# Optimization experiments

Measured on AMD Instinct MI355X. Metric: run time of the kernel, lower is better.

## Reference

```python
import jax, jax.numpy as jnp
import numpy as np
from jax import lax

D_MODEL = 1024
STATE_DIM = 32
GROUPS = 8
GROUP_DIM = D_MODEL // GROUPS
DT_MIN = 0.001
DT_MAX = 0.1
EPS = 1e-6


def setup_inputs() -> dict:
    key = jax.random.key(0)
    ks = jax.random.split(key, 6)
    B, T = 4, 4096
    u = jax.random.normal(ks[0], (B, T, D_MODEL), dtype=jnp.float32)
    state = jnp.zeros((B, GROUPS, STATE_DIM), dtype=jnp.float32)
    A_log = jax.random.normal(ks[1], (GROUPS, STATE_DIM), dtype=jnp.float32) * 0.02
    B_param = jax.random.normal(ks[2], (GROUPS, STATE_DIM, GROUP_DIM), dtype=jnp.float32) * 0.02
    C = jax.random.normal(ks[3], (GROUPS, GROUP_DIM, STATE_DIM), dtype=jnp.float32) * 0.02
    Dp = jnp.zeros((GROUPS, GROUP_DIM), dtype=jnp.float32)
    dt_logit = jnp.zeros((GROUPS,), dtype=jnp.float32)
    return {"u": u, "state": state, "A_log": A_log, "B_param": B_param,
            "C": C, "Dp": Dp, "dt_logit": dt_logit}


def reference(u, state, A_log, B_param, C, Dp, dt_logit):
    Bsz, T, Dm = u.shape
    A = -jax.nn.softplus(A_log)                                  # [G,N]
    dt = DT_MIN + (DT_MAX - DT_MIN) * jax.nn.sigmoid(dt_logit)   # [G]
    dt_g = dt[:, None]                                           # [G,1]
    Abar = jnp.exp(A * dt_g)                                     # [G,N]
    # (exp(A dt) - 1)/A, stable for small |A|
    frac = jnp.where(jnp.abs(A) > EPS, (Abar - 1.0) / A,
                     jnp.broadcast_to(dt_g, A.shape))            # [G,N]
    Bbar = frac[..., None] * B_param                             # [G,N,gd]

    u_g = u.reshape(Bsz, T, GROUPS, GROUP_DIM)                   # [B,T,G,gd]
    # precompute input injections for all timesteps, then scan the LTI recurrence
    Bu = jnp.einsum('btgi,gni->btgn', u_g, Bbar)                 # [B,T,G,N]
    Bu_t = jnp.moveaxis(Bu, 1, 0)                                # [T,B,G,N]

    def step(s, bu):
        s = s * Abar + bu                                        # [B,G,N]
        return s, s

    s_final, states = lax.scan(step, state, Bu_t)                # states: [T,B,G,N]
    Cs = jnp.einsum('tbgn,gdn->btgd', states, C)                 # [B,T,G,gd]
    y = (Cs + Dp * u_g).reshape(Bsz, T, Dm)                      # [B,T,D]
    return y, s_final
```

## Files before the change

### kernel.cpp

```cpp
#include <hip/hip_runtime.h>
#include <hip/hip_bf16.h>

#define DM 1024
#define SD 32
#define NG 8
#define GD 128
#define BS 4
#define TT 4096
#define CL 64
#define NC (TT/CL)

typedef __attribute__((ext_vector_type(8))) short short8;
typedef __attribute__((ext_vector_type(4))) float f32x4;

#define WS_POWA  0
#define WS_STL   65536
#define WS_CARRY (WS_STL + 8388608)
#define WS_PAL   (WS_CARRY + 262144)

__device__ __forceinline__ unsigned short f2bf(float f) {
  __hip_bfloat16 h = __float2bfloat16(f);
  return __builtin_bit_cast(unsigned short, h);
}
__device__ __forceinline__ float bf2f(unsigned short h) {
  return __uint_as_float(((unsigned)h) << 16);
}
__device__ __forceinline__ float softplus_f(float x) {
  return (x > 20.f) ? x : log1pf(expf(x));
}
__device__ __forceinline__ short8 pack8(float4 a, float4 b) {
  short8 h;
  h[0]=(short)f2bf(a.x); h[1]=(short)f2bf(a.y); h[2]=(short)f2bf(a.z); h[3]=(short)f2bf(a.w);
  h[4]=(short)f2bf(b.x); h[5]=(short)f2bf(b.y); h[6]=(short)f2bf(b.z); h[7]=(short)f2bf(b.w);
  return h;
}

__global__ __launch_bounds__(64) void ka_bu_scan(const float* __restrict__ u,
                                                 const float* __restrict__ A_log,
                                                 const float* __restrict__ B_param,
                                                 const float* __restrict__ dt_logit,
                                                 unsigned char* __restrict__ ws) {
  const int bx = blockIdx.x;
  const int c = bx & (NC - 1);
  const int g = (bx >> 6) & (NG - 1);
  const int b = bx >> 9;
  const int l = threadIdx.x;
  const int lr = l & 15, lh = l >> 4;

  const float dtg = 0.001f + 0.099f * (1.f / (1.f + expf(-dt_logit[g])));

  float fracv[2];
  #pragma unroll
  for (int nt = 0; nt < 2; ++nt) {
    int n = nt * 16 + lr;
    float A = -softplus_f(A_log[g * SD + n]);
    float a = expf(A * dtg);
    fracv[nt] = (fabsf(A) > 1e-6f) ? (a - 1.f) / A : dtg;
  }
  float a_scan;
  {
    float A = -softplus_f(A_log[g * SD + (l & 31)]);
    a_scan = expf(A * dtg);
  }

  const float* bp = B_param + (size_t)g * SD * GD;
  short8 bfr[4][2];
  #pragma unroll
  for (int kt = 0; kt < 4; ++kt)
    #pragma unroll
    for (int nt = 0; nt < 2; ++nt) {
      const float* p = bp + (size_t)(nt * 16 + lr) * GD + kt * 32 + lh * 8;
      float4 v0 = *(const float4*)p;
      float4 v1 = *(const float4*)(p + 4);
      float s = fracv[nt];
      v0.x*=s; v0.y*=s; v0.z*=s; v0.w*=s;
      v1.x*=s; v1.y*=s; v1.z*=s; v1.w*=s;
      bfr[kt][nt] = pack8(v0, v1);
    }

  const float* up = u + ((size_t)b * TT + (size_t)c * CL) * DM + g * GD;
  float4 ub[2][4][2];
  #pragma unroll
  for (int kt = 0; kt < 2; ++kt)
    #pragma unroll
    for (int m = 0; m < 4; ++m) {
      const float* p = up + (size_t)(m * 16 + lr) * DM + kt * 32 + lh * 8;
      ub[kt][m][0] = *(const float4*)p;
      ub[kt][m][1] = *(const float4*)(p + 4);
    }

  f32x4 acc[4][2];
  #pragma unroll
  for (int m = 0; m < 4; ++m)
    #pragma unroll
    for (int nt = 0; nt < 2; ++nt)
      #pragma unroll
      for (int j = 0; j < 4; ++j) acc[m][nt][j] = 0.f;

  #pragma unroll
  for (int kt = 0; kt < 4; ++kt) {
    short8 af[4];
    #pragma unroll
    for (int m = 0; m < 4; ++m)
      af[m] = pack8(ub[kt & 1][m][0], ub[kt & 1][m][1]);
    if (kt < 2) {
      #pragma unroll
      for (int m = 0; m < 4; ++m) {
        const float* p = up + (size_t)(m * 16 + lr) * DM + (kt + 2) * 32 + lh * 8;
        ub[kt & 1][m][0] = *(const float4*)p;
        ub[kt & 1][m][1] = *(const float4*)(p + 4);
      }
    }
    #pragma unroll
    for (int m = 0; m < 4; ++m)
      #pragma unroll
      for (int nt = 0; nt < 2; ++nt)
        acc[m][nt] = __builtin_amdgcn_mfma_f32_16x16x32_bf16(af[m], bfr[kt][nt], acc[m][nt], 0, 0, 0);
  }

  __shared__ __align__(16) float sBu[CL * 33];
  __shared__ __align__(16) unsigned short sSt[CL * SD];
  #pragma unroll
  for (int m = 0; m < 4; ++m)
    #pragma unroll
    for (int nt = 0; nt < 2; ++nt)
      #pragma unroll
      for (int j = 0; j < 4; ++j) {
        int t = m * 16 + lh * 4 + j;
        sBu[t * 33 + (nt * 16 + lr)] = acc[m][nt][j];
      }
  __syncthreads();

  float* carry = (float*)(ws + WS_CARRY);
  if (l < SD) {
    float s = 0.f;
    #pragma unroll
    for (int t = 0; t < CL; ++t) {
      s = fmaf(s, a_scan, sBu[t * 33 + l]);
      sSt[t * SD + l] = f2bf(s);
    }
    carry[((b * NG + g) * NC + c) * SD + l] = s;
  }
  __syncthreads();

  unsigned short* stg = (unsigned short*)(ws + WS_STL) + ((size_t)((b * NC + c) * NG + g)) * CL * SD;
  #pragma unroll
  for (int p = 0; p < 4; ++p) {
    int off = (p * 64 + l) * 8;
    *(short8*)(stg + off) = *(short8*)(sSt + off);
  }

  if (b == 0 && c == 0 && l < SD) {
    float* powA = (float*)(ws + WS_POWA);
    float* powAL = (float*)(ws + WS_PAL);
    float p = 1.f;
    #pragma unroll
    for (int t = 0; t < CL; ++t) {
      p *= a_scan;
      powA[(g * CL + t) * SD + l] = p;
    }
    float aL = p;
    float q = 1.f;
    #pragma unroll
    for (int j = 0; j < CL; ++j) {
      powAL[(g * CL + j) * SD + l] = q;
      q *= aL;
    }
  }
}

__global__ __launch_bounds__(128) void kb_y(const float* __restrict__ u,
                                            const float* __restrict__ state0,
                                            const float* __restrict__ C,
                                            const float* __restrict__ Dp,
                                            unsigned char* __restrict__ ws,
                                            float* __restrict__ y,
                                            float* __restrict__ sfin) {
  const int bx = blockIdx.x;
  const int c = bx & (NC - 1);
  const int g = (bx >> 6) & (NG - 1);
  const int b = bx >> 9;
  const int tid = threadIdx.x;
  const int w = tid >> 6;
  const int l = tid & 63;
  const int lr = l & 15, lh = l >> 4;
  const int n = l & 31;

  const float* powA = (const float*)(ws + WS_POWA) + g * CL * SD;
  const float* powAL = (const float*)(ws + WS_PAL) + g * CL * SD;
  const float* carry = (const float*)(ws + WS_CARRY) + (size_t)(b * NG + g) * NC * SD;
  const unsigned short* stg = (const unsigned short*)(ws + WS_STL) + ((size_t)((b * NC + c) * NG + g)) * CL * SD;

  bool need_u;
  {
    float2 dpc = *(const float2*)(Dp + g * GD + l * 2);
    need_u = __ballot((dpc.x != 0.f) || (dpc.y != 0.f)) != 0ULL;
  }

  float p;
  {
    float a0 = 0.f, a1 = 0.f, a2 = 0.f, a3 = 0.f;
    int cc = 0;
    while (cc + 8 <= c) {
      float ca[8], wt[8];
      #pragma unroll
      for (int e = 0; e < 8; ++e) {
        ca[e] = carry[(cc + e) * SD + n];
        wt[e] = powAL[(c - 1 - cc - e) * SD + n];
      }
      a0 = fmaf(wt[0], ca[0], a0); a1 = fmaf(wt[1], ca[1], a1);
      a2 = fmaf(wt[2], ca[2], a2); a3 = fmaf(wt[3], ca[3], a3);
      a0 = fmaf(wt[4], ca[4], a0); a1 = fmaf(wt[5], ca[5], a1);
      a2 = fmaf(wt[6], ca[6], a2); a3 = fmaf(wt[7], ca[7], a3);
      cc += 8;
    }
    for (; cc < c; ++cc)
      a0 = fmaf(powAL[(c - 1 - cc) * SD + n], carry[cc * SD + n], a0);
    p = fmaf(state0[(b * NG + g) * SD + n], powAL[c * SD + n], (a0 + a1) + (a2 + a3));
  }
  if (w == 0 && c == NC - 1 && l < SD) {
    const float aL = powA[(CL - 1) * SD + l];
    sfin[(b * NG + g) * SD + l] = fmaf(p, aL, carry[(NC - 1) * SD + l]);
  }

  float pr[8];
  #pragma unroll
  for (int e = 0; e < 8; ++e) pr[e] = __shfl(p, lh * 8 + e);

  short8 sf[4];
  #pragma unroll
  for (int tt = 0; tt < 4; ++tt) {
    int t = tt * 16 + lr;
    short8 sl = *(const short8*)(stg + t * SD + lh * 8);
    const float* pw = powA + t * SD + lh * 8;
    float4 pw0 = *(const float4*)pw;
    float4 pw1 = *(const float4*)(pw + 4);
    short8 hh;
    hh[0] = (short)f2bf(bf2f((unsigned short)sl[0]) + pw0.x * pr[0]);
    hh[1] = (short)f2bf(bf2f((unsigned short)sl[1]) + pw0.y * pr[1]);
    hh[2] = (short)f2bf(bf2f((unsigned short)sl[2]) + pw0.z * pr[2]);
    hh[3] = (short)f2bf(bf2f((unsigned short)sl[3]) + pw0.w * pr[3]);
    hh[4] = (short)f2bf(bf2f((unsigned short)sl[4]) + pw1.x * pr[4]);
    hh[5] = (short)f2bf(bf2f((unsigned short)sl[5]) + pw1.y * pr[5]);
    hh[6] = (short)f2bf(bf2f((unsigned short)sl[6]) + pw1.z * pr[6]);
    hh[7] = (short)f2bf(bf2f((unsigned short)sl[7]) + pw1.w * pr[7]);
    sf[tt] = hh;
  }

  const float* cp = C + (size_t)g * GD * SD;
  const size_t rowbase = ((size_t)b * TT + (size_t)c * CL) * DM + g * GD;

  short8 cf[4];
  #pragma unroll
  for (int dd = 0; dd < 4; ++dd) {
    int d = (w * 4 + dd) * 16 + lr;
    const float* pp = cp + (size_t)d * SD + lh * 8;
    float4 v0 = *(const float4*)pp;
    float4 v1 = *(const float4*)(pp + 4);
    cf[dd] = pack8(v0, v1);
  }
  f32x4 acc[4][4];
  #pragma unroll
  for (int dd = 0; dd < 4; ++dd)
    #pragma unroll
    for (int tt = 0; tt < 4; ++tt) {
      f32x4 z;
      #pragma unroll
      for (int j = 0; j < 4; ++j) z[j] = 0.f;
      acc[dd][tt] = __builtin_amdgcn_mfma_f32_16x16x32_bf16(cf[dd], sf[tt], z, 0, 0, 0);
    }

  #pragma unroll
  for (int dd = 0; dd < 4; ++dd) {
    int d0 = (w * 4 + dd) * 16 + lh * 4;
    float4 dp4 = *(const float4*)(Dp + g * GD + d0);
    #pragma unroll
    for (int tt = 0; tt < 4; ++tt) {
      int t = tt * 16 + lr;
      size_t off = rowbase + (size_t)t * DM + d0;
      float4 r;
      r.x = acc[dd][tt][0]; r.y = acc[dd][tt][1];
      r.z = acc[dd][tt][2]; r.w = acc[dd][tt][3];
      if (need_u) {
        float4 u4 = *(const float4*)(u + off);
        r.x += dp4.x * u4.x; r.y += dp4.y * u4.y;
        r.z += dp4.z * u4.z; r.w += dp4.w * u4.w;
      }
      *(float4*)(y + off) = r;
    }
  }
}

extern "C" void kernel_launch(void* const* d_in, const int* in_sizes, int n_in,
                              void* d_out, int out_size, void* d_ws, size_t ws_size,
                              hipStream_t stream) {
  const float* u       = (const float*)d_in[0];
  const float* state0  = (const float*)d_in[1];
  const float* A_log   = (const float*)d_in[2];
  const float* B_param = (const float*)d_in[3];
  const float* C       = (const float*)d_in[4];
  const float* Dp      = (const float*)d_in[5];
  const float* dtl     = (const float*)d_in[6];
  float* y = (float*)d_out;
  unsigned char* ws = (unsigned char*)d_ws;
  float* sfin = y + (size_t)BS * TT * DM;

  ka_bu_scan<<<dim3(BS * NG * NC), dim3(64), 0, stream>>>(u, A_log, B_param, dtl, ws);
  kb_y<<<dim3(BS * NG * NC), dim3(128), 0, stream>>>(u, state0, C, Dp, ws, y, sfin);
}
```

Baseline: 45.88 us.

## Restructure output kernel to write full contiguous rows via LDS staging

The output kernel now assigns one 512-thread block to 16 timesteps across all 8 groups, with each wave handling one group. MFMA results are staged through shared memory so full 1024-float rows of y are written contiguously, instead of scattered 128-float group slices. The scan kernel's block index order is also changed so groups vary fastest. The tradeoff is that each block recomputes the carry prefix per group for every 16-timestep quarter, and adds LDS traffic plus block-level barriers.

Measured after the change: 52.26 us. 13.9% more time.

```diff
diff --git a/kernel.cpp b/kernel.cpp
--- a/kernel.cpp
+++ b/kernel.cpp
@@ -41,8 +41,8 @@
                                                  const float* __restrict__ dt_logit,
                                                  unsigned char* __restrict__ ws) {
   const int bx = blockIdx.x;
-  const int c = bx & (NC - 1);
-  const int g = (bx >> 6) & (NG - 1);
+  const int g = bx & (NG - 1);
+  const int c = (bx >> 3) & (NC - 1);
   const int b = bx >> 9;
   const int l = threadIdx.x;
   const int lr = l & 15, lh = l >> 4;
@@ -169,7 +169,7 @@
   }
 }
 
-__global__ __launch_bounds__(128) void kb_y(const float* __restrict__ u,
+__global__ __launch_bounds__(512) void kb_y(const float* __restrict__ u,
                                             const float* __restrict__ state0,
                                             const float* __restrict__ C,
                                             const float* __restrict__ Dp,
@@ -177,11 +177,11 @@
                                             float* __restrict__ y,
                                             float* __restrict__ sfin) {
   const int bx = blockIdx.x;
-  const int c = bx & (NC - 1);
-  const int g = (bx >> 6) & (NG - 1);
-  const int b = bx >> 9;
+  const int tq = bx & 3;
+  const int c = (bx >> 2) & (NC - 1);
+  const int b = bx >> 8;
   const int tid = threadIdx.x;
-  const int w = tid >> 6;
+  const int g = tid >> 6;
   const int l = tid & 63;
   const int lr = l & 15, lh = l >> 4;
   const int n = l & 31;
@@ -191,10 +191,14 @@
   const float* carry = (const float*)(ws + WS_CARRY) + (size_t)(b * NG + g) * NC * SD;
   const unsigned short* stg = (const unsigned short*)(ws + WS_STL) + ((size_t)((b * NC + c) * NG + g)) * CL * SD;
 
-  bool need_u;
+  __shared__ __align__(16) float sY[8 * 1028];
+  __shared__ int sNeed;
+
+  if (tid == 0) sNeed = 0;
+  __syncthreads();
   {
-    float2 dpc = *(const float2*)(Dp + g * GD + l * 2);
-    need_u = __ballot((dpc.x != 0.f) || (dpc.y != 0.f)) != 0ULL;
+    float2 dpc = *(const float2*)(Dp + tid * 2);
+    if (dpc.x != 0.f || dpc.y != 0.f) sNeed = 1;
   }
 
   float p;
@@ -218,7 +222,7 @@
       a0 = fmaf(powAL[(c - 1 - cc) * SD + n], carry[cc * SD + n], a0);
     p = fmaf(state0[(b * NG + g) * SD + n], powAL[c * SD + n], (a0 + a1) + (a2 + a3));
   }
-  if (w == 0 && c == NC - 1 && l < SD) {
+  if (tq == 0 && c == NC - 1 && l < SD) {
     const float aL = powA[(CL - 1) * SD + l];
     sfin[(b * NG + g) * SD + l] = fmaf(p, aL, carry[(NC - 1) * SD + l]);
   }
@@ -227,66 +231,68 @@
   #pragma unroll
   for (int e = 0; e < 8; ++e) pr[e] = __shfl(p, lh * 8 + e);
 
-  short8 sf[4];
-  #pragma unroll
-  for (int tt = 0; tt < 4; ++tt) {
-    int t = tt * 16 + lr;
+  short8 sf;
+  {
+    const int t = tq * 16 + lr;
     short8 sl = *(const short8*)(stg + t * SD + lh * 8);
     const float* pw = powA + t * SD + lh * 8;
     float4 pw0 = *(const float4*)pw;
     float4 pw1 = *(const float4*)(pw + 4);
-    short8 hh;
-    hh[0] = (short)f2bf(bf2f((unsigned short)sl[0]) + pw0.x * pr[0]);
-    hh[1] = (short)f2bf(bf2f((unsigned short)sl[1]) + pw0.y * pr[1]);
-    hh[2] = (short)f2bf(bf2f((unsigned short)sl[2]) + pw0.z * pr[2]);
-    hh[3] = (short)f2bf(bf2f((unsigned short)sl[3]) + pw0.w * pr[3]);
-    hh[4] = (short)f2bf(bf2f((unsigned short)sl[4]) + pw1.x * pr[4]);
-    hh[5] = (short)f2bf(bf2f((unsigned short)sl[5]) + pw1.y * pr[5]);
-    hh[6] = (short)f2bf(bf2f((unsigned short)sl[6]) + pw1.z * pr[6]);
-    hh[7] = (short)f2bf(bf2f((unsigned short)sl[7]) + pw1.w * pr[7]);
-    sf[tt] = hh;
+    sf[0] = (short)f2bf(bf2f((unsigned short)sl[0]) + pw0.x * pr[0]);
+    sf[1] = (short)f2bf(bf2f((unsigned short)sl[1]) + pw0.y * pr[1]);
+    sf[2] = (short)f2bf(bf2f((unsigned short)sl[2]) + pw0.z * pr[2]);
+    sf[3] = (short)f2bf(bf2f((unsigned short)sl[3]) + pw0.w * pr[3]);
+    sf[4] = (short)f2bf(bf2f((unsigned short)sl[4]) + pw1.x * pr[4]);
+    sf[5] = (short)f2bf(bf2f((unsigned short)sl[5]) + pw1.y * pr[5]);
+    sf[6] = (short)f2bf(bf2f((unsigned short)sl[6]) + pw1.z * pr[6]);
+    sf[7] = (short)f2bf(bf2f((unsigned short)sl[7]) + pw1.w * pr[7]);
   }
 
   const float* cp = C + (size_t)g * GD * SD;
-  const size_t rowbase = ((size_t)b * TT + (size_t)c * CL) * DM + g * GD;
-
-  short8 cf[4];
-  #pragma unroll
-  for (int dd = 0; dd < 4; ++dd) {
-    int d = (w * 4 + dd) * 16 + lr;
+  f32x4 acc[8];
+  #pragma unroll
+  for (int dt = 0; dt < 8; ++dt) {
+    int d = dt * 16 + lr;
     const float* pp = cp + (size_t)d * SD + lh * 8;
     float4 v0 = *(const float4*)pp;
     float4 v1 = *(const float4*)(pp + 4);
-    cf[dd] = pack8(v0, v1);
-  }
-  f32x4 acc[4][4];
-  #pragma unroll
-  for (int dd = 0; dd < 4; ++dd)
-    #pragma unroll
-    for (int tt = 0; tt < 4; ++tt) {
-      f32x4 z;
-      #pragma unroll
-      for (int j = 0; j < 4; ++j) z[j] = 0.f;
-      acc[dd][tt] = __builtin_amdgcn_mfma_f32_16x16x32_bf16(cf[dd], sf[tt], z, 0, 0, 0);
-    }
-
-  #pragma unroll
-  for (int dd = 0; dd < 4; ++dd) {
-    int d0 = (w * 4 + dd) * 16 + lh * 4;
-    float4 dp4 = *(const float4*)(Dp + g * GD + d0);
-    #pragma unroll
-    for (int tt = 0; tt < 4; ++tt) {
-      int t = tt * 16 + lr;
-      size_t off = rowbase + (size_t)t * DM + d0;
-      float4 r;
-      r.x = acc[dd][tt][0]; r.y = acc[dd][tt][1];
-      r.z = acc[dd][tt][2]; r.w = acc[dd][tt][3];
-      if (need_u) {
+    short8 cf = pack8(v0, v1);
+    f32x4 z;
+    #pragma unroll
+    for (int j = 0; j < 4; ++j) z[j] = 0.f;
+    acc[dt] = __builtin_amdgcn_mfma_f32_16x16x32_bf16(cf, sf, z, 0, 0, 0);
+  }
+
+  __syncthreads();
+  const bool need = (sNeed != 0);
+  const size_t slabbase = ((size_t)b * TT + (size_t)c * CL + (size_t)tq * 16) * DM;
+
+  #pragma unroll
+  for (int sp = 0; sp < 2; ++sp) {
+    if (sp) __syncthreads();
+    if ((lr >> 3) == sp) {
+      const int row = lr & 7;
+      #pragma unroll
+      for (int dt = 0; dt < 8; ++dt) {
+        int d0 = g * GD + dt * 16 + lh * 4;
+        *(float4*)(sY + row * 1028 + d0) = (float4){acc[dt][0], acc[dt][1], acc[dt][2], acc[dt][3]};
+      }
+    }
+    __syncthreads();
+    #pragma unroll
+    for (int r = 0; r < 4; ++r) {
+      int flat = r * 512 + tid;
+      int row = flat >> 8;
+      int c4 = (flat & 255) * 4;
+      f32x4 v = *(const f32x4*)(sY + row * 1028 + c4);
+      size_t off = slabbase + (size_t)(sp * 8 + row) * DM + c4;
+      if (need) {
         float4 u4 = *(const float4*)(u + off);
-        r.x += dp4.x * u4.x; r.y += dp4.y * u4.y;
-        r.z += dp4.z * u4.z; r.w += dp4.w * u4.w;
-      }
-      *(float4*)(y + off) = r;
+        float4 dp4 = *(const float4*)(Dp + c4);
+        v[0] += dp4.x * u4.x; v[1] += dp4.y * u4.y;
+        v[2] += dp4.z * u4.z; v[3] += dp4.w * u4.w;
+      }
+      *(f32x4*)(y + off) = v;
     }
   }
 }
@@ -306,5 +312,5 @@
   float* sfin = y + (size_t)BS * TT * DM;
 
   ka_bu_scan<<<dim3(BS * NG * NC), dim3(64), 0, stream>>>(u, A_log, B_param, dtl, ws);
-  kb_y<<<dim3(BS * NG * NC), dim3(128), 0, stream>>>(u, state0, C, Dp, ws, y, sfin);
-}
+  kb_y<<<dim3(BS * NC * 4), dim3(512), 0, stream>>>(u, state0, C, Dp, ws, y, sfin);
+}
```
